# Kernel tuning notes

Measured on AMD Instinct MI355X. Metric: run time of the kernel, lower is better.

## Reference

```python
import jax, jax.numpy as jnp
import numpy as np

N = 96                       # max_num_nodes
T = N * (N + 1) // 2         # upper-triangular vector length
E = 256                      # embedding_dim
MAX_ITERS = 50


def setup_inputs() -> dict:
    key = jax.random.key(0)
    ks = jax.random.split(key, 8)
    graph_embedding = jax.random.normal(ks[0], (1, E), jnp.float32)
    a = (jax.random.uniform(ks[1], (1, N, N)) < 0.1).astype(jnp.float32)
    adj = jnp.maximum(a, jnp.swapaxes(a, 1, 2))  # symmetric 0/1 adjacency
    mask = jnp.ones((1, N), bool)
    W1 = jax.random.normal(ks[2], (E, 250), jnp.float32) * 0.08
    b1 = jnp.zeros((250,), jnp.float32)
    W2 = jax.random.normal(ks[3], (250, 100), jnp.float32) * 0.10
    b2 = jnp.zeros((100,), jnp.float32)
    W3 = jax.random.normal(ks[4], (100, T), jnp.float32) * 0.15
    b3 = jnp.zeros((T,), jnp.float32)
    return dict(graph_embedding=graph_embedding, adj=adj, mask=mask,
                W1=W1, b1=b1, W2=W2, b2=b2, W3=W3, b3=b3)


def _forward(graph_embedding, adj, mask, W1, b1, W2, b2, W3, b3):
    idx = jnp.arange(N)
    eye = jnp.eye(N, dtype=adj.dtype)

    # decoder: Linear -> Linear -> ReLU -> Linear -> sigmoid
    h = graph_embedding @ W1 + b1
    h = jax.nn.relu(h @ W2 + b2)
    l = jax.nn.sigmoid(h @ W3 + b3)[0]              # [T]

    # recover_adj_lower + recover_full_adj_from_lower
    iu = jnp.triu_indices(N)
    up = jnp.zeros((N, N), l.dtype).at[iu].set(l)    # row-major triu fill, as torch bool-mask assign
    recon = up + up.T - jnp.diag(jnp.diag(up))       # [N, N]
    fr = recon.sum(axis=1)                           # recon degree features

    # ori_adj with diagonal forced to 1 where mask
    a0 = adj[0]
    m = mask[0]
    ori = a0.at[idx, idx].set(jnp.where(m, jnp.asarray(1.0, a0.dtype), jnp.diag(a0)))
    f = ori.sum(axis=1)                              # ori degree features

    # edge_similarity_matrix, vectorized
    # off-diagonal block: S[i,j,a,b] = A[i,j]A[i,i]A[j,j] * R[a,b]R[a,a]R[b,b]  (i!=j, a!=b)
    dA = jnp.diag(ori)
    dR = jnp.diag(recon)
    t1 = (1.0 - eye) * ori * dA[:, None] * dA[None, :]      # [N, N], zero on diag
    t2 = (1.0 - eye) * recon * dR[:, None] * dR[None, :]    # [N, N], zero on diag
    S = t1[:, :, None, None] * t2[None, None, :, :]          # [N, N, N, N]
    # diagonal block: S[i,i,a,a] = A[i,i]R[a,a] / (|f_i - fr_a| + 1)
    sim = 1.0 / (jnp.abs(f[:, None] - fr[None, :]) + 1.0)    # [N, N]
    D = dA[:, None] * dR[None, :] * sim                      # [N, N]
    S = S.at[idx[:, None], idx[:, None], idx[None, :], idx[None, :]].set(D)

    # mpm: iterative max-pooling matching
    x0 = jnp.full((N, N), 1.0 / N, dtype=S.dtype)
    off_mask = (1.0 - eye)[:, :, None]                       # exclude j == i

    def step(x, _):
        pooled = jnp.max(x[None, :, None, :] * S, axis=3)    # [i, j, a] = max_b x[j,b]*S[i,j,a,b]
        neigh = (off_mask * pooled).sum(axis=1)              # [i, a]
        x_new = x * D + neigh                                # D[i,a] == S[i,i,a,a]
        x_new = x_new / jnp.linalg.norm(x_new)
        return x_new, None

    x, _ = jax.lax.scan(step, x0, None, length=MAX_ITERS)
    return x  # soft assignment matrix [N, N]


def reference(graph_embedding, adj, mask, W1, b1, W2, b2, W3, b3):
    return _forward(graph_embedding, adj, mask, W1, b1, W2, b2, W3, b3)
```

## Files before the change

kernel.cpp:

```cpp
#include <hip/hip_runtime.h>
#include <hip/hip_bf16.h>

#define NN 96
#define NB 32
#define NTH 256
#define RPB 3
#define NITER 50
#define SMASK 0x8000000080000000ULL
#define SPIN_MAX 32768
#define MAXF 32

typedef unsigned long long ull;
typedef float v2f __attribute__((ext_vector_type(2)));

__device__ __forceinline__ float bf2f(__hip_bfloat16 v){ return __bfloat162float(v); }
__device__ __forceinline__ float LD(const void* p, int i, bool f32){
  return f32 ? ((const float*)p)[i]
             : __bfloat162float(((const __hip_bfloat16*)p)[i]);
}
__device__ __forceinline__ float ldA(const float* p){
  return __hip_atomic_load(p, __ATOMIC_RELAXED, __HIP_MEMORY_SCOPE_AGENT);
}
__device__ __forceinline__ void stA(float* p, float v){
  __hip_atomic_store(p, v, __ATOMIC_RELAXED, __HIP_MEMORY_SCOPE_AGENT);
}
__device__ __forceinline__ ull ldA64(const ull* p){
  return __hip_atomic_load(p, __ATOMIC_RELAXED, __HIP_MEMORY_SCOPE_AGENT);
}
__device__ __forceinline__ void stA64(ull* p, ull v){
  __hip_atomic_store(p, v, __ATOMIC_RELAXED, __HIP_MEMORY_SCOPE_AGENT);
}
__device__ __forceinline__ int ldSacq(const int* p){
  return __hip_atomic_load(p, __ATOMIC_ACQUIRE, __HIP_MEMORY_SCOPE_WORKGROUP);
}
__device__ __forceinline__ void stSrel(int* p, int v){
  __hip_atomic_store(p, v, __ATOMIC_RELEASE, __HIP_MEMORY_SCOPE_WORKGROUP);
}

__global__ __launch_bounds__(NTH, 1) void gvae(
    const void* __restrict__ ge,  const void* __restrict__ adj,
    const void* __restrict__ W1,  const void* __restrict__ b1,
    const void* __restrict__ W2,  const void* __restrict__ b2,
    const void* __restrict__ W3,  const void* __restrict__ b3,
    void* __restrict__ out, float* __restrict__ ws)
{
  __shared__ __align__(16) float t2s[NN * NN + 4600];
  __shared__ __align__(16) float stg[4656];
  __shared__ __align__(16) float xs[RPB * NN];
  __shared__ __align__(16) float Ds[RPB * NN];
  __shared__ __align__(16) float msd[4 * RPB * NN];
  __shared__ float ges[256], h1s[250], h2s[100];
  __shared__ unsigned char nbl[RPB * 96];
  __shared__ unsigned char onbl[RPB * 2];
  __shared__ int   fcnts[RPB], ocnts[RPB];
  __shared__ float fdeg[RPB];
  __shared__ float frs[NN], dRs[NN];
  __shared__ float wpart[4 * RPB];
  __shared__ int   wpstamp[4 * RPB];
  __shared__ int   rstamp[4 * RPB];
  __shared__ float sring[8];
  __shared__ int   sstamp[8];
  __shared__ int   bdone;

  const int tid = threadIdx.x, blk = blockIdx.x;

  float* pn  = ws;
  float* lg  = ws + 2048;
  ull*   Mb0 = (ull*)(ws + 8192);
  ull*   Mb1 = Mb0 + 4608;

  if (blk >= NB){
    if (tid == 0) bdone = 0;
    __syncthreads();
    const float* dn = ws + 1664;
    const int wv = tid >> 6;
    float a0 = 1.1f + blk, a1 = 2.2f, a2 = 3.3f, a3 = 4.4f;
    float a4 = 5.5f, a5 = 6.6f, a6 = 7.7f, a7 = 8.8f;
    const float m = 1.0000001f;
    for (int outer = 0; outer < 16384; ++outer){
#pragma unroll
      for (int u = 0; u < 8; ++u){
        a0 = fmaf(a0, m, 1e-6f); a1 = fmaf(a1, m, 2e-6f);
        a2 = fmaf(a2, m, 3e-6f); a3 = fmaf(a3, m, 4e-6f);
        a4 = fmaf(a4, m, 5e-6f); a5 = fmaf(a5, m, 6e-6f);
        a6 = fmaf(a6, m, 7e-6f); a7 = fmaf(a7, m, 8e-6f);
      }
      __builtin_amdgcn_s_sleep(4);
      int stop;
      if (wv == 0){
        float v = (tid == 0 && (outer & 7) == 0) ? ldA(dn) : 0.f;
        stop = __any(v > 0.5f) ? 1 : 0;
        if (stop && tid == 0)
          __hip_atomic_store(&bdone, 1, __ATOMIC_RELAXED, __HIP_MEMORY_SCOPE_WORKGROUP);
      } else {
        stop = __hip_atomic_load(&bdone, __ATOMIC_RELAXED, __HIP_MEMORY_SCOPE_WORKGROUP);
      }
      if (stop) break;
    }
    float sum = a0 + a1 + a2 + a3 + a4 + a5 + a6 + a7;
    if (sum == 0.12345678f) stA(ws + 1700, sum);
    return;
  }

  float sv = (tid < 128) ? bf2f(((const __hip_bfloat16*)W1)[tid])
                         : bf2f(((const __hip_bfloat16*)W3)[tid - 128]);
  const bool isf32 = __syncthreads_or(!(fabsf(sv) < 1e4f)) != 0;

  if (tid < 256) ges[tid] = LD(ge, tid, isf32);
  __syncthreads();
  if (tid < 250){
    float a0 = LD(b1, tid, isf32), a1 = 0.f, a2 = 0.f, a3 = 0.f;
    for (int e = 0; e < 256; e += 4){
      a0 += ges[e]     * LD(W1, (e    ) * 250 + tid, isf32);
      a1 += ges[e + 1] * LD(W1, (e + 1) * 250 + tid, isf32);
      a2 += ges[e + 2] * LD(W1, (e + 2) * 250 + tid, isf32);
      a3 += ges[e + 3] * LD(W1, (e + 3) * 250 + tid, isf32);
    }
    h1s[tid] = (a0 + a1) + (a2 + a3);
  }
  __syncthreads();
  if (tid < 100){
    float a0 = LD(b2, tid, isf32), a1 = 0.f;
    for (int k = 0; k < 250; k += 2){
      a0 += h1s[k]     * LD(W2, (k    ) * 100 + tid, isf32);
      a1 += h1s[k + 1] * LD(W2, (k + 1) * 100 + tid, isf32);
    }
    h2s[tid] = fmaxf(a0 + a1, 0.f);
  }
  __syncthreads();

  if (tid < 146){
    int o = blk * 146 + tid;
    if (o < 4656){
      float a = LD(b3, o, isf32);
      for (int k = 0; k < 100; ++k) a += h2s[k] * LD(W3, k * 4656 + o, isf32);
      stA(&lg[o], 1.f / (1.f + expf(-a)));
    }
  }
  if (tid >= 192 && tid < 192 + RPB){
    int r = tid - 192, ig = blk * RPB + r;
    int lo = blk * RPB, hi = lo + RPB;
    float fs = 1.f; int c = 0, co = 0;
    for (int j = 0; j < NN; ++j){
      if (j == ig) continue;
      float v = LD(adj, ig * NN + j, isf32);
      fs += v;
      if (v > 0.5f){
        if (j >= lo && j < hi) onbl[r * 2 + (co++)] = (unsigned char)(j - lo);
        else                   nbl[r * 96 + (c++)]  = (unsigned char)j;
      }
    }
    fcnts[r] = c; ocnts[r] = co; fdeg[r] = fs;
  }
  {
    float vv[19];
    unsigned pend = 0;
#pragma unroll
    for (int c = 0; c < 19; ++c) if (tid + NTH * c < 4656) pend |= 1u << c;
    int spin = 0;
    while (pend && spin++ < SPIN_MAX){
      unsigned p2 = pend;
#pragma unroll
      for (int c = 0; c < 19; ++c)
        if ((p2 >> c) & 1) vv[c] = ldA(&lg[tid + NTH * c]);
#pragma unroll
      for (int c = 0; c < 19; ++c)
        if (((p2 >> c) & 1) && vv[c] > 0.f){
          stg[tid + NTH * c] = vv[c];
          pend &= ~(1u << c);
        }
      if (pend == p2) __builtin_amdgcn_s_sleep(2);
    }
  }
  __syncthreads();

  for (int e = tid; e < NN * NN; e += NTH){
    int a = e / NN, b = e % NN, i = min(a, b), j = max(a, b);
    int k = i * NN - (i * (i - 1)) / 2 + (j - i);
    t2s[e] = stg[k];
  }
  __syncthreads();
  if (tid < NN){
    float srow = 0.f;
    for (int b = 0; b < NN; ++b) srow += t2s[b * NN + tid];
    frs[tid] = srow; dRs[tid] = t2s[tid * NN + tid];
  }
  __syncthreads();
  for (int e = tid; e < NN * NN; e += NTH){
    int a = e / NN, b = e % NN;
    t2s[e] = (a == b) ? 0.f : t2s[e] * dRs[a] * dRs[b];
  }
  for (int o = tid; o < RPB * NN; o += NTH){
    int r = o / NN, a = o % NN;
    Ds[o] = dRs[a] / (fabsf(fdeg[r] - frs[a]) + 1.f);
    xs[o] = 1.f / 96.f;
  }
  if (tid < 4 * RPB){ rstamp[tid] = -1; wpstamp[tid] = -1; }
  if (tid < 8) sstamp[tid] = -1;
  __syncthreads();

  const int wv = tid >> 6, l = tid & 63;

  if (wv < RPB){
    const int g = blk * RPB + wv;
    const bool act = (l < 48);
    const int p = l;
    int fc = 0, nf = 0, gw = 0;
    int off[MAXF];
    const int oc  = ocnts[wv];
    const int ow0 = onbl[wv * 2], ow1 = onbl[wv * 2 + 1];
    if (act){
      fc = fcnts[wv]; nf = fc < MAXF ? fc : MAXF;
      gw = g * 48 + p;
#pragma unroll
      for (int c = 0; c < MAXF; ++c)
        off[c] = (c < nf) ? ((int)nbl[wv * 96 + c] * 48 + p) : gw;
    }

    for (int it = 0; it < NITER; ++it){
      ull* Mw = (it & 1) ? Mb1 : Mb0;
      const ull sg = ((it >> 1) & 1) ? SMASK : 0ULL;
      const int ring = (it & 3) * RPB;

      float mx = 0.f, my = 0.f;
      if (act){
        v2f m0 = {0.f, 0.f}, m1 = {0.f, 0.f};
        v2f m2 = {0.f, 0.f}, m3 = {0.f, 0.f};
        for (int b = 0; b < NN; b += 4){
          v2f t0 = *(const v2f*)&t2s[(b    ) * NN + 2 * p];
          v2f t1 = *(const v2f*)&t2s[(b + 1) * NN + 2 * p];
          v2f t2 = *(const v2f*)&t2s[(b + 2) * NN + 2 * p];
          v2f t3 = *(const v2f*)&t2s[(b + 3) * NN + 2 * p];
          v2f xv = *(const v2f*)&xs[wv * NN + b];
          v2f xw = *(const v2f*)&xs[wv * NN + b + 2];
          m0.x = fmaxf(m0.x, xv.x * t0.x); m0.y = fmaxf(m0.y, xv.x * t0.y);
          m1.x = fmaxf(m1.x, xv.y * t1.x); m1.y = fmaxf(m1.y, xv.y * t1.y);
          m2.x = fmaxf(m2.x, xw.x * t2.x); m2.y = fmaxf(m2.y, xw.x * t2.y);
          m3.x = fmaxf(m3.x, xw.y * t3.x); m3.y = fmaxf(m3.y, xw.y * t3.y);
        }
        mx = fmaxf(fmaxf(m0.x, m1.x), fmaxf(m2.x, m3.x));
        my = fmaxf(fmaxf(m0.y, m1.y), fmaxf(m2.y, m3.y));
        *(v2f*)&msd[(ring + wv) * NN + 2 * p] = (v2f){mx, my};
      }
      if (l == 0) stSrel(&rstamp[ring + wv], it);
      if (act){
        ull enc = (((ull)__float_as_uint(my + 1.f)) << 32) | __float_as_uint(mx + 1.f);
        stA64(&Mw[gw], enc ^ sg);
      }

      float s = 1.f;
      if (it >= 2){
        int sl = it & 7, sp = 0;
        while (ldSacq(&sstamp[sl]) != it && ++sp < SPIN_MAX)
          if ((sp & 63) == 0) __builtin_amdgcn_s_sleep(1);
        s = sring[sl];
      }

      v2f acc = {0.f, 0.f};
      if (act){
        ull vv[MAXF];
        unsigned pend = (nf >= 32) ? 0xffffffffu : ((1u << nf) - 1u);
        int spin = 0;
        while (pend && spin++ < SPIN_MAX){
          unsigned p2 = pend;
#pragma unroll
          for (int c = 0; c < MAXF; ++c)
            if ((p2 >> c) & 1) vv[c] = ldA64(&Mw[off[c]]);
#pragma unroll
          for (int c = 0; c < MAXF; ++c)
            if (((p2 >> c) & 1) && !((vv[c] ^ sg) & SMASK)) pend &= ~(1u << c);
        }
#pragma unroll
        for (int c = 0; c < MAXF; ++c)
          if (c < nf){
            acc.x += fabsf(__uint_as_float((unsigned)vv[c])) - 1.f;
            acc.y += fabsf(__uint_as_float((unsigned)(vv[c] >> 32))) - 1.f;
          }
        for (int c = MAXF; c < fc; ++c){
          int o3 = (int)nbl[wv * 96 + c] * 48 + p;
          ull w; int sp = 0;
          do { w = ldA64(&Mw[o3]); } while (((w ^ sg) & SMASK) && ++sp < SPIN_MAX);
          acc.x += fabsf(__uint_as_float((unsigned)w)) - 1.f;
          acc.y += fabsf(__uint_as_float((unsigned)(w >> 32))) - 1.f;
        }
      }
      for (int t = 0; t < oc; ++t){
        int wj = (t == 0) ? ow0 : ow1;
        int rs = ring + wj, sp = 0;
        while (ldSacq(&rstamp[rs]) != it && ++sp < SPIN_MAX){}
        if (act){
          v2f mv = *(const v2f*)&msd[rs * NN + 2 * p];
          acc.x += mv.x; acc.y += mv.y;
        }
      }

      float nsq = 0.f;
      if (act){
        v2f w2 = *(const v2f*)&xs[wv * NN + 2 * p];
        v2f d2 = *(const v2f*)&Ds[wv * NN + 2 * p];
        v2f u; u.x = s * (w2.x * d2.x + acc.x); u.y = s * (w2.y * d2.y + acc.y);
        *(v2f*)&xs[wv * NN + 2 * p] = u;
        nsq = u.x * u.x + u.y * u.y;
      }
      for (int o2 = 32; o2; o2 >>= 1) nsq += __shfl_down(nsq, o2, 64);
      if (l == 0){
        wpart[ring + wv] = nsq;
        stSrel(&wpstamp[ring + wv], it);
      }
    }
  } else {
    for (int it = 0; it <= NITER; ++it){
      if (l == 0 && it >= 1){
        int sl = ((it - 1) & 3) * RPB; float t = 0.f;
        for (int w = 0; w < RPB; ++w){
          int sp = 0;
          while (ldSacq(&wpstamp[sl + w]) != it - 1 && ++sp < SPIN_MAX)
            if ((sp & 63) == 0) __builtin_amdgcn_s_sleep(1);
          t += wpart[sl + w];
        }
        stA(&pn[it * NB + blk], t);
      }
      if (it >= 2){
        int slot = (it == NITER) ? NITER : (it - 1);
        float v = 0.f;
        if (l < NB){
          int sp = 0;
          for (;;){
            v = ldA(&pn[slot * NB + l]);
            if (v > 0.f || ++sp >= SPIN_MAX) break;
            __builtin_amdgcn_s_sleep(1);
          }
        }
        for (int o2 = 16; o2; o2 >>= 1) v += __shfl_down(v, o2, 64);
        if (l == 0){
          sring[it & 7] = rsqrtf(v);
          stSrel(&sstamp[it & 7], it);
        }
      }
    }
  }
  __syncthreads();

  float sf = sring[NITER & 7];
  for (int o = tid; o < RPB * NN; o += NTH){
    int og = blk * RPB * NN + o;
    float v = sf * xs[o];
    if (isf32) ((float*)out)[og] = v;
    else       ((__hip_bfloat16*)out)[og] = __float2bfloat16(v);
  }
  if (blk == 0 && tid == 0) stA(ws + 1664, 1.f);
}

extern "C" void kernel_launch(void* const* d_in, const int* in_sizes, int n_in,
                              void* d_out, int out_size, void* d_ws, size_t ws_size,
                              hipStream_t stream) {
  (void)in_sizes; (void)n_in; (void)out_size; (void)ws_size;
  hipLaunchKernelGGL(gvae, dim3(256), dim3(NTH), 0, stream,
                     d_in[0], d_in[1], d_in[3], d_in[4], d_in[5], d_in[6],
                     d_in[7], d_in[8], d_out, (float*)d_ws);
}
```

Baseline: 407.7 us.

## Spread matching rows across 96 single-row blocks instead of 32 three-row blocks

Changes the persistent kernel's work split from 32 blocks of 256 threads, each owning 3 rows, to 96 blocks of 128 threads, each owning one row. This removes the intra-block shared-memory neighbour exchange (msd/rstamp) and its stamp waits. Every neighbour max-pool contribution now goes through global memory, and the per-iteration norm reduction has to poll 96 partials instead of 32. The aim is more parallel cores working on the per-iteration max-pool, at the cost of more cross-block global traffic and larger synchronisation fan-in.

```diff
diff --git a/kernel.cpp b/kernel.cpp
--- a/kernel.cpp
+++ b/kernel.cpp
@@ -2,9 +2,8 @@
 #include <hip/hip_bf16.h>
 
 #define NN 96
-#define NB 32
-#define NTH 256
-#define RPB 3
+#define NB 96
+#define NTH 128
 #define NITER 50
 #define SMASK 0x8000000080000000ULL
 #define SPIN_MAX 32768
@@ -44,20 +43,17 @@
     const void* __restrict__ W3,  const void* __restrict__ b3,
     void* __restrict__ out, float* __restrict__ ws)
 {
-  __shared__ __align__(16) float t2s[NN * NN + 4600];
+  __shared__ __align__(16) float t2s[NN * NN + 5700];
   __shared__ __align__(16) float stg[4656];
-  __shared__ __align__(16) float xs[RPB * NN];
-  __shared__ __align__(16) float Ds[RPB * NN];
-  __shared__ __align__(16) float msd[4 * RPB * NN];
+  __shared__ __align__(16) float xs[NN];
+  __shared__ __align__(16) float Ds[NN];
   __shared__ float ges[256], h1s[250], h2s[100];
-  __shared__ unsigned char nbl[RPB * 96];
-  __shared__ unsigned char onbl[RPB * 2];
-  __shared__ int   fcnts[RPB], ocnts[RPB];
-  __shared__ float fdeg[RPB];
+  __shared__ unsigned char nbl[NN];
+  __shared__ int   fcnt;
+  __shared__ float fdeg1;
   __shared__ float frs[NN], dRs[NN];
-  __shared__ float wpart[4 * RPB];
-  __shared__ int   wpstamp[4 * RPB];
-  __shared__ int   rstamp[4 * RPB];
+  __shared__ float wpart[4];
+  __shared__ int   wpstamp[4];
   __shared__ float sring[8];
   __shared__ int   sstamp[8];
   __shared__ int   bdone;
@@ -65,14 +61,14 @@
   const int tid = threadIdx.x, blk = blockIdx.x;
 
   float* pn  = ws;
-  float* lg  = ws + 2048;
-  ull*   Mb0 = (ull*)(ws + 8192);
+  float* lg  = ws + 5120;
+  ull*   Mb0 = (ull*)(ws + 10240);
   ull*   Mb1 = Mb0 + 4608;
 
   if (blk >= NB){
     if (tid == 0) bdone = 0;
     __syncthreads();
-    const float* dn = ws + 1664;
+    const float* dn = ws + 4960;
     const int wv = tid >> 6;
     float a0 = 1.1f + blk, a1 = 2.2f, a2 = 3.3f, a3 = 4.4f;
     float a4 = 5.5f, a5 = 6.6f, a6 = 7.7f, a7 = 8.8f;
@@ -98,25 +94,25 @@
       if (stop) break;
     }
     float sum = a0 + a1 + a2 + a3 + a4 + a5 + a6 + a7;
-    if (sum == 0.12345678f) stA(ws + 1700, sum);
+    if (sum == 0.12345678f) stA(ws + 4992, sum);
     return;
   }
 
-  float sv = (tid < 128) ? bf2f(((const __hip_bfloat16*)W1)[tid])
-                         : bf2f(((const __hip_bfloat16*)W3)[tid - 128]);
+  float sv = bf2f(((const __hip_bfloat16*)W1)[tid]);
   const bool isf32 = __syncthreads_or(!(fabsf(sv) < 1e4f)) != 0;
 
-  if (tid < 256) ges[tid] = LD(ge, tid, isf32);
-  __syncthreads();
-  if (tid < 250){
-    float a0 = LD(b1, tid, isf32), a1 = 0.f, a2 = 0.f, a3 = 0.f;
+  ges[tid] = LD(ge, tid, isf32);
+  ges[tid + 128] = LD(ge, tid + 128, isf32);
+  __syncthreads();
+  for (int o = tid; o < 250; o += NTH){
+    float a0 = LD(b1, o, isf32), a1 = 0.f, a2 = 0.f, a3 = 0.f;
     for (int e = 0; e < 256; e += 4){
-      a0 += ges[e]     * LD(W1, (e    ) * 250 + tid, isf32);
-      a1 += ges[e + 1] * LD(W1, (e + 1) * 250 + tid, isf32);
-      a2 += ges[e + 2] * LD(W1, (e + 2) * 250 + tid, isf32);
-      a3 += ges[e + 3] * LD(W1, (e + 3) * 250 + tid, isf32);
-    }
-    h1s[tid] = (a0 + a1) + (a2 + a3);
+      a0 += ges[e]     * LD(W1, (e    ) * 250 + o, isf32);
+      a1 += ges[e + 1] * LD(W1, (e + 1) * 250 + o, isf32);
+      a2 += ges[e + 2] * LD(W1, (e + 2) * 250 + o, isf32);
+      a3 += ges[e + 3] * LD(W1, (e + 3) * 250 + o, isf32);
+    }
+    h1s[o] = (a0 + a1) + (a2 + a3);
   }
   __syncthreads();
   if (tid < 100){
@@ -129,45 +125,40 @@
   }
   __syncthreads();
 
-  if (tid < 146){
-    int o = blk * 146 + tid;
+  if (tid < 49){
+    int o = blk * 49 + tid;
     if (o < 4656){
       float a = LD(b3, o, isf32);
       for (int k = 0; k < 100; ++k) a += h2s[k] * LD(W3, k * 4656 + o, isf32);
       stA(&lg[o], 1.f / (1.f + expf(-a)));
     }
   }
-  if (tid >= 192 && tid < 192 + RPB){
-    int r = tid - 192, ig = blk * RPB + r;
-    int lo = blk * RPB, hi = lo + RPB;
-    float fs = 1.f; int c = 0, co = 0;
+  if (tid == 64){
+    float fs = 1.f; int c = 0;
     for (int j = 0; j < NN; ++j){
-      if (j == ig) continue;
-      float v = LD(adj, ig * NN + j, isf32);
+      if (j == blk) continue;
+      float v = LD(adj, blk * NN + j, isf32);
       fs += v;
-      if (v > 0.5f){
-        if (j >= lo && j < hi) onbl[r * 2 + (co++)] = (unsigned char)(j - lo);
-        else                   nbl[r * 96 + (c++)]  = (unsigned char)j;
-      }
-    }
-    fcnts[r] = c; ocnts[r] = co; fdeg[r] = fs;
+      if (v > 0.5f) nbl[c++] = (unsigned char)j;
+    }
+    fcnt = c; fdeg1 = fs;
   }
   {
-    float vv[19];
-    unsigned pend = 0;
-#pragma unroll
-    for (int c = 0; c < 19; ++c) if (tid + NTH * c < 4656) pend |= 1u << c;
+    float vv[37];
+    ull pend = 0;
+#pragma unroll
+    for (int c = 0; c < 37; ++c) if (tid + NTH * c < 4656) pend |= 1ull << c;
     int spin = 0;
     while (pend && spin++ < SPIN_MAX){
-      unsigned p2 = pend;
-#pragma unroll
-      for (int c = 0; c < 19; ++c)
+      ull p2 = pend;
+#pragma unroll
+      for (int c = 0; c < 37; ++c)
         if ((p2 >> c) & 1) vv[c] = ldA(&lg[tid + NTH * c]);
 #pragma unroll
-      for (int c = 0; c < 19; ++c)
+      for (int c = 0; c < 37; ++c)
         if (((p2 >> c) & 1) && vv[c] > 0.f){
           stg[tid + NTH * c] = vv[c];
-          pend &= ~(1u << c);
+          pend &= ~(1ull << c);
         }
       if (pend == p2) __builtin_amdgcn_s_sleep(2);
     }
@@ -190,37 +181,32 @@
     int a = e / NN, b = e % NN;
     t2s[e] = (a == b) ? 0.f : t2s[e] * dRs[a] * dRs[b];
   }
-  for (int o = tid; o < RPB * NN; o += NTH){
-    int r = o / NN, a = o % NN;
-    Ds[o] = dRs[a] / (fabsf(fdeg[r] - frs[a]) + 1.f);
-    xs[o] = 1.f / 96.f;
-  }
-  if (tid < 4 * RPB){ rstamp[tid] = -1; wpstamp[tid] = -1; }
+  if (tid < NN){
+    Ds[tid] = dRs[tid] / (fabsf(fdeg1 - frs[tid]) + 1.f);
+    xs[tid] = 1.f / 96.f;
+  }
+  if (tid < 4) wpstamp[tid] = -1;
   if (tid < 8) sstamp[tid] = -1;
   __syncthreads();
 
   const int wv = tid >> 6, l = tid & 63;
 
-  if (wv < RPB){
-    const int g = blk * RPB + wv;
+  if (wv == 0){
     const bool act = (l < 48);
     const int p = l;
     int fc = 0, nf = 0, gw = 0;
     int off[MAXF];
-    const int oc  = ocnts[wv];
-    const int ow0 = onbl[wv * 2], ow1 = onbl[wv * 2 + 1];
     if (act){
-      fc = fcnts[wv]; nf = fc < MAXF ? fc : MAXF;
-      gw = g * 48 + p;
+      fc = fcnt; nf = fc < MAXF ? fc : MAXF;
+      gw = blk * 48 + p;
 #pragma unroll
       for (int c = 0; c < MAXF; ++c)
-        off[c] = (c < nf) ? ((int)nbl[wv * 96 + c] * 48 + p) : gw;
+        off[c] = (c < nf) ? ((int)nbl[c] * 48 + p) : gw;
     }
 
     for (int it = 0; it < NITER; ++it){
       ull* Mw = (it & 1) ? Mb1 : Mb0;
       const ull sg = ((it >> 1) & 1) ? SMASK : 0ULL;
-      const int ring = (it & 3) * RPB;
 
       float mx = 0.f, my = 0.f;
       if (act){
@@ -231,8 +217,8 @@
           v2f t1 = *(const v2f*)&t2s[(b + 1) * NN + 2 * p];
           v2f t2 = *(const v2f*)&t2s[(b + 2) * NN + 2 * p];
           v2f t3 = *(const v2f*)&t2s[(b + 3) * NN + 2 * p];
-          v2f xv = *(const v2f*)&xs[wv * NN + b];
-          v2f xw = *(const v2f*)&xs[wv * NN + b + 2];
+          v2f xv = *(const v2f*)&xs[b];
+          v2f xw = *(const v2f*)&xs[b + 2];
           m0.x = fmaxf(m0.x, xv.x * t0.x); m0.y = fmaxf(m0.y, xv.x * t0.y);
           m1.x = fmaxf(m1.x, xv.y * t1.x); m1.y = fmaxf(m1.y, xv.y * t1.y);
           m2.x = fmaxf(m2.x, xw.x * t2.x); m2.y = fmaxf(m2.y, xw.x * t2.y);
@@ -240,10 +226,6 @@
         }
         mx = fmaxf(fmaxf(m0.x, m1.x), fmaxf(m2.x, m3.x));
         my = fmaxf(fmaxf(m0.y, m1.y), fmaxf(m2.y, m3.y));
-        *(v2f*)&msd[(ring + wv) * NN + 2 * p] = (v2f){mx, my};
-      }
-      if (l == 0) stSrel(&rstamp[ring + wv], it);
-      if (act){
         ull enc = (((ull)__float_as_uint(my + 1.f)) << 32) | __float_as_uint(mx + 1.f);
         stA64(&Mw[gw], enc ^ sg);
       }
@@ -277,61 +259,57 @@
             acc.y += fabsf(__uint_as_float((unsigned)(vv[c] >> 32))) - 1.f;
           }
         for (int c = MAXF; c < fc; ++c){
-          int o3 = (int)nbl[wv * 96 + c] * 48 + p;
+          int o3 = (int)nbl[c] * 48 + p;
           ull w; int sp = 0;
           do { w = ldA64(&Mw[o3]); } while (((w ^ sg) & SMASK) && ++sp < SPIN_MAX);
           acc.x += fabsf(__uint_as_float((unsigned)w)) - 1.f;
           acc.y += fabsf(__uint_as_float((unsigned)(w >> 32))) - 1.f;
         }
       }
-      for (int t = 0; t < oc; ++t){
-        int wj = (t == 0) ? ow0 : ow1;
-        int rs = ring + wj, sp = 0;
-        while (ldSacq(&rstamp[rs]) != it && ++sp < SPIN_MAX){}
-        if (act){
-          v2f mv = *(const v2f*)&msd[rs * NN + 2 * p];
-          acc.x += mv.x; acc.y += mv.y;
-        }
-      }
 
       float nsq = 0.f;
       if (act){
-        v2f w2 = *(const v2f*)&xs[wv * NN + 2 * p];
-        v2f d2 = *(const v2f*)&Ds[wv * NN + 2 * p];
+        v2f w2 = *(const v2f*)&xs[2 * p];
+        v2f d2 = *(const v2f*)&Ds[2 * p];
         v2f u; u.x = s * (w2.x * d2.x + acc.x); u.y = s * (w2.y * d2.y + acc.y);
-        *(v2f*)&xs[wv * NN + 2 * p] = u;
+        *(v2f*)&xs[2 * p] = u;
         nsq = u.x * u.x + u.y * u.y;
       }
       for (int o2 = 32; o2; o2 >>= 1) nsq += __shfl_down(nsq, o2, 64);
       if (l == 0){
-        wpart[ring + wv] = nsq;
-        stSrel(&wpstamp[ring + wv], it);
+        wpart[it & 3] = nsq;
+        stSrel(&wpstamp[it & 3], it);
       }
     }
   } else {
     for (int it = 0; it <= NITER; ++it){
       if (l == 0 && it >= 1){
-        int sl = ((it - 1) & 3) * RPB; float t = 0.f;
-        for (int w = 0; w < RPB; ++w){
-          int sp = 0;
-          while (ldSacq(&wpstamp[sl + w]) != it - 1 && ++sp < SPIN_MAX)
-            if ((sp & 63) == 0) __builtin_amdgcn_s_sleep(1);
-          t += wpart[sl + w];
-        }
-        stA(&pn[it * NB + blk], t);
+        int sl = (it - 1) & 3, sp = 0;
+        while (ldSacq(&wpstamp[sl]) != it - 1 && ++sp < SPIN_MAX)
+          if ((sp & 63) == 0) __builtin_amdgcn_s_sleep(1);
+        stA(&pn[it * NB + blk], wpart[sl]);
       }
       if (it >= 2){
         int slot = (it == NITER) ? NITER : (it - 1);
-        float v = 0.f;
-        if (l < NB){
+        float va = 0.f, vb = 0.f;
+        {
           int sp = 0;
           for (;;){
-            v = ldA(&pn[slot * NB + l]);
-            if (v > 0.f || ++sp >= SPIN_MAX) break;
+            va = ldA(&pn[slot * NB + l]);
+            if (va > 0.f || ++sp >= SPIN_MAX) break;
             __builtin_amdgcn_s_sleep(1);
           }
         }
-        for (int o2 = 16; o2; o2 >>= 1) v += __shfl_down(v, o2, 64);
+        if (l < 32){
+          int sp = 0;
+          for (;;){
+            vb = ldA(&pn[slot * NB + 64 + l]);
+            if (vb > 0.f || ++sp >= SPIN_MAX) break;
+            __builtin_amdgcn_s_sleep(1);
+          }
+        }
+        float v = va + vb;
+        for (int o2 = 32; o2; o2 >>= 1) v += __shfl_down(v, o2, 64);
         if (l == 0){
           sring[it & 7] = rsqrtf(v);
           stSrel(&sstamp[it & 7], it);
@@ -342,13 +320,13 @@
   __syncthreads();
 
   float sf = sring[NITER & 7];
-  for (int o = tid; o < RPB * NN; o += NTH){
-    int og = blk * RPB * NN + o;
-    float v = sf * xs[o];
+  if (tid < NN){
+    float v = sf * xs[tid];
+    int og = blk * NN + tid;
     if (isf32) ((float*)out)[og] = v;
     else       ((__hip_bfloat16*)out)[og] = __float2bfloat16(v);
   }
-  if (blk == 0 && tid == 0) stA(ws + 1664, 1.f);
+  if (blk == 0 && tid == 0) stA(ws + 4960, 1.f);
 }
 
 extern "C" void kernel_launch(void* const* d_in, const int* in_sizes, int n_in,
```

Measured after the change: 415.6 us. Within noise of the previous version (+1.9%).
